# Optimization experiments

Hardware: AMD Instinct MI355X
Metric: run time of the kernel (lower is better)

## Reference

```python
import jax, jax.numpy as jnp
import numpy as np

SEQ_LEN, INPUT_DIM, HIDDEN, CLASSES, BATCH = 512, 512, 1024, 1000, 256


def _xavier(key, shape):
    fan_in, fan_out = shape
    limit = float(np.sqrt(6.0 / (fan_in + fan_out)))
    return jax.random.uniform(key, shape, jnp.float32, -limit, limit)


def setup_inputs() -> dict:
    key = jax.random.key(0)
    ks = jax.random.split(key, 10)
    inp = {
        "x": jax.random.normal(ks[0], (BATCH, INPUT_DIM, SEQ_LEN), jnp.float32),
        "W_fx": _xavier(ks[1], (INPUT_DIM, HIDDEN)),
        "W_fh": _xavier(ks[2], (HIDDEN, HIDDEN)),
        "W_gx": _xavier(ks[3], (INPUT_DIM, HIDDEN)),
        "W_gh": _xavier(ks[4], (HIDDEN, HIDDEN)),
        "W_ix": _xavier(ks[5], (INPUT_DIM, HIDDEN)),
        "W_ih": _xavier(ks[6], (HIDDEN, HIDDEN)),
        "W_ox": _xavier(ks[7], (INPUT_DIM, HIDDEN)),
        "W_oh": _xavier(ks[8], (HIDDEN, HIDDEN)),
        "W_ph": _xavier(ks[9], (HIDDEN, CLASSES)),
        "b_f": jnp.zeros((HIDDEN,), jnp.float32),
        "b_g": jnp.zeros((HIDDEN,), jnp.float32),
        "b_i": jnp.zeros((HIDDEN,), jnp.float32),
        "b_o": jnp.zeros((HIDDEN,), jnp.float32),
        "b_p": jnp.zeros((CLASSES,), jnp.float32),
    }
    return inp


def _lstm_forward(x, W_fx, W_fh, W_gx, W_gh, W_ix, W_ih, W_ox, W_oh,
                  W_ph, b_f, b_g, b_i, b_o, b_p):
    B, D, T = x.shape
    H = W_fh.shape[0]
    # Fuse the four input projections into one GEMM: [T, B, 4H]
    Wx = jnp.concatenate([W_gx, W_fx, W_ix, W_ox], axis=1)      # [D, 4H]
    Wh = jnp.concatenate([W_gh, W_fh, W_ih, W_oh], axis=1)      # [H, 4H]
    bias = jnp.concatenate([b_g, b_f, b_i, b_o])                # [4H]
    xt = jnp.transpose(x, (2, 0, 1))                            # [T, B, D]
    xproj = jnp.einsum('tbd,de->tbe', xt, Wx) + bias            # [T, B, 4H]

    def step(carry, xp):
        h, c = carry
        gates = jnp.tanh(h @ Wh + xp)                           # NOTE: source uses tanh for ALL gates
        g, f, i, o = jnp.split(gates, 4, axis=-1)
        c = g * i + c * f
        h = jnp.tanh(c) * o
        return (h, c), None

    h0 = jnp.zeros((B, H), x.dtype)
    c0 = jnp.zeros((B, H), x.dtype)
    (h, _), _ = jax.lax.scan(step, (h0, c0), xproj)
    return jax.nn.softmax(h @ W_ph + b_p, axis=-1)


def reference(x, W_fx, W_fh, W_gx, W_gh, W_ix, W_ih, W_ox, W_oh,
              W_ph, b_f, b_g, b_i, b_o, b_p):
    return _lstm_forward(x, W_fx, W_fh, W_gx, W_gh, W_ix, W_ih, W_ox, W_oh,
                         W_ph, b_f, b_g, b_i, b_o, b_p)
```

## Files before the change

### kernel.cpp

```cpp
#include <hip/hip_runtime.h>

#define B_SZ   256
#define D_IN   512
#define T_LEN  512
#define H_DIM  1024
#define KTOT   1536
#define NCLASS 1000

using half8   = __attribute__((ext_vector_type(8))) _Float16;
using floatx4 = __attribute__((ext_vector_type(4))) float;

__device__ __forceinline__ float ftanh(float x) {
    x = fminf(fmaxf(x, -20.f), 20.f);
    float e = __expf(2.f * x);
    return (e - 1.f) / (e + 1.f);
}

__global__ void k_transpose_x(const float* __restrict__ x, _Float16* __restrict__ xT) {
    __shared__ float tile[32][33];
    int b = blockIdx.z, d0 = blockIdx.y * 32, t0 = blockIdx.x * 32;
    int tx = threadIdx.x, ty = threadIdx.y;
    const float* xp = x + ((size_t)b * D_IN + d0) * T_LEN + t0;
#pragma unroll
    for (int i = 0; i < 4; ++i)
        tile[ty + i * 8][tx] = xp[(size_t)(ty + i * 8) * T_LEN + tx];
    __syncthreads();
#pragma unroll
    for (int i = 0; i < 4; ++i) {
        int t = t0 + ty + i * 8;
        xT[((size_t)t * B_SZ + b) * D_IN + d0 + tx] = (_Float16)tile[tx][ty + i * 8];
    }
}

__global__ void k_build_wcat(const float* __restrict__ Wgh, const float* __restrict__ Wfh,
                             const float* __restrict__ Wih, const float* __restrict__ Woh,
                             const float* __restrict__ Wgx, const float* __restrict__ Wfx,
                             const float* __restrict__ Wix, const float* __restrict__ Wox,
                             _Float16* __restrict__ WcatT) {
    int src = blockIdx.z;
    int kmax = (src < 4) ? 1024 : 512;
    int koff = (src < 4) ? 0 : 1024;
    int gi = src & 3;
    const float* W;
    switch (src) {
        case 0: W = Wgh; break; case 1: W = Wfh; break;
        case 2: W = Wih; break; case 3: W = Woh; break;
        case 4: W = Wgx; break; case 5: W = Wfx; break;
        case 6: W = Wix; break; default: W = Wox; break;
    }
    int k0 = blockIdx.y * 32;
    if (k0 >= kmax) return;
    int j0 = blockIdx.x * 32;
    __shared__ float tile[32][33];
    int tx = threadIdx.x, ty = threadIdx.y;
#pragma unroll
    for (int i = 0; i < 4; ++i)
        tile[ty + i * 8][tx] = W[(size_t)(k0 + ty + i * 8) * 1024 + j0 + tx];
    __syncthreads();
#pragma unroll
    for (int i = 0; i < 4; ++i) {
        int n = gi * 1024 + j0 + ty + i * 8;
        WcatT[(size_t)n * KTOT + koff + k0 + tx] = (_Float16)tile[tx][ty + i * 8];
    }
}

__global__ void k_init(float* __restrict__ c, unsigned int* __restrict__ h0u,
                       float* __restrict__ bias,
                       const float* __restrict__ bg, const float* __restrict__ bf,
                       const float* __restrict__ bi, const float* __restrict__ bo) {
    int idx = blockIdx.x * 256 + threadIdx.x;
    if (idx < 262144) c[idx] = 0.f;
    if (idx < 131072) h0u[idx] = 0u;
    if (idx < 4096) {
        int gi = idx >> 10, j = idx & 1023;
        float v = (gi == 0) ? bg[j] : (gi == 1) ? bf[j] : (gi == 2) ? bi[j] : bo[j];
        bias[idx] = v;
    }
}

__device__ __forceinline__ void bar() {
    asm volatile("s_waitcnt lgkmcnt(0)" ::: "memory");
    __builtin_amdgcn_s_barrier();
    asm volatile("" ::: "memory");
}

__global__ __launch_bounds__(256)
void k_step(const _Float16* __restrict__ h_in, _Float16* __restrict__ h_out,
            float* __restrict__ h_f32, float* __restrict__ c_st,
            const _Float16* __restrict__ xTt, const _Float16* __restrict__ WcatT,
            const float* __restrict__ bias, int is_last) {
    __shared__ __align__(16) _Float16 As[2][64][72];
    __shared__ __align__(16) _Float16 Bs[2][64][72];

    int bid = blockIdx.x;
    int xcd = bid & 7, idx = bid >> 3;
    int cg = xcd * 8 + (idx & 7);
    int rg = idx >> 3;
    int r0 = rg * 64, hc0 = cg * 16;

    int tid = threadIdx.x, wave = tid >> 6, lane = tid & 63;

    floatx4 acc[4];
#pragma unroll
    for (int g = 0; g < 4; ++g) acc[g] = (floatx4){0.f, 0.f, 0.f, 0.f};

    int arow = tid >> 2, ac16 = (tid & 3) << 4;
    const _Float16* hbase = h_in + (size_t)(r0 + arow) * H_DIM + ac16;
    const _Float16* xbase = xTt + (size_t)(r0 + arow) * D_IN + ac16;
    const _Float16* bbase = WcatT +
        (size_t)((arow >> 4) * 1024 + hc0 + (arow & 15)) * KTOT + ac16;

    int am = wave * 16 + (lane & 15);
    int koffA = (lane >> 4) << 3;
    int ncol = lane & 15;

#define LOADSET(A0, A1, B0, B1, c) do {                                         \
        const _Float16* _sa = ((c) < 16) ? (hbase + ((c) << 6))                 \
                                         : (xbase + (((c) - 16) << 6));         \
        A0 = ((const uint4*)_sa)[0]; A1 = ((const uint4*)_sa)[1];               \
        const _Float16* _sb = bbase + ((c) << 6);                               \
        B0 = ((const uint4*)_sb)[0]; B1 = ((const uint4*)_sb)[1];               \
    } while (0)

#define STORESET(A0, A1, B0, B1, buf) do {                                      \
        *(uint4*)&As[buf][arow][ac16]     = A0;                                 \
        *(uint4*)&As[buf][arow][ac16 + 8] = A1;                                 \
        *(uint4*)&Bs[buf][arow][ac16]     = B0;                                 \
        *(uint4*)&Bs[buf][arow][ac16 + 8] = B1;                                 \
    } while (0)

#define MFMA_CHUNK(buf) do {                                                    \
        _Pragma("unroll")                                                       \
        for (int kk = 0; kk < 2; ++kk) {                                        \
            half8 af = *(const half8*)&As[buf][am][kk * 32 + koffA];            \
            _Pragma("unroll")                                                   \
            for (int g = 0; g < 4; ++g) {                                       \
                half8 bf8 = *(const half8*)&Bs[buf][g * 16 + ncol][kk * 32 + koffA]; \
                acc[g] = __builtin_amdgcn_mfma_f32_16x16x32_f16(af, bf8, acc[g], 0, 0, 0); \
            }                                                                   \
        }                                                                       \
    } while (0)

    uint4 aA0, aA1, bA0, bA1;
    uint4 aB0, aB1, bB0, bB1;

    LOADSET(aA0, aA1, bA0, bA1, 0);
    LOADSET(aB0, aB1, bB0, bB1, 1);
    STORESET(aA0, aA1, bA0, bA1, 0);
    LOADSET(aA0, aA1, bA0, bA1, 2);
    bar();

#pragma unroll
    for (int cc = 0; cc < 12; ++cc) {
        STORESET(aB0, aB1, bB0, bB1, 1);
        MFMA_CHUNK(0);
        if (2 * cc + 3 < 24) LOADSET(aB0, aB1, bB0, bB1, 2 * cc + 3);
        bar();
        if (2 * cc + 2 < 24) STORESET(aA0, aA1, bA0, bA1, 0);
        MFMA_CHUNK(1);
        if (2 * cc + 4 < 24) LOADSET(aA0, aA1, bA0, bA1, 2 * cc + 4);
        bar();
    }

#undef LOADSET
#undef STORESET
#undef MFMA_CHUNK

    int q = lane >> 4, col = lane & 15;
    int gcol = hc0 + col;
    float bg_ = bias[gcol], bf_ = bias[1024 + gcol];
    float bi_ = bias[2048 + gcol], bo_ = bias[3072 + gcol];
#pragma unroll
    for (int r = 0; r < 4; ++r) {
        int grow = r0 + wave * 16 + q * 4 + r;
        size_t off = (size_t)grow * H_DIM + gcol;
        float g  = ftanh(acc[0][r] + bg_);
        float f  = ftanh(acc[1][r] + bf_);
        float ii = ftanh(acc[2][r] + bi_);
        float o  = ftanh(acc[3][r] + bo_);
        float cn = g * ii + c_st[off] * f;
        c_st[off] = cn;
        float hn = ftanh(cn) * o;
        h_out[off] = (_Float16)hn;
        if (is_last) h_f32[off] = hn;
    }
}

__global__ void k_logits(const float* __restrict__ h, const float* __restrict__ Wp,
                         const float* __restrict__ bp, float* __restrict__ logits) {
    __shared__ float hs[32][65];
    int r0 = blockIdx.y * 32;
    int c0 = blockIdx.x * 64;
    int tid = threadIdx.x;
    int wave = tid >> 6, tx = tid & 63;
    int col = c0 + tx;
    float s[8];
#pragma unroll
    for (int i = 0; i < 8; ++i) s[i] = 0.f;
    for (int kc = 0; kc < 16; ++kc) {
        int k0 = kc * 64;
#pragma unroll
        for (int i = 0; i < 8; ++i) {
            int idx = tid + i * 256;
            hs[idx >> 6][idx & 63] = h[(size_t)(r0 + (idx >> 6)) * H_DIM + k0 + (idx & 63)];
        }
        __syncthreads();
        if (col < NCLASS) {
            for (int kk = 0; kk < 64; ++kk) {
                float wv = Wp[(size_t)(k0 + kk) * NCLASS + col];
#pragma unroll
                for (int rr = 0; rr < 8; ++rr) s[rr] += hs[wave * 8 + rr][kk] * wv;
            }
        }
        __syncthreads();
    }
    if (col < NCLASS) {
#pragma unroll
        for (int rr = 0; rr < 8; ++rr)
            logits[(size_t)(r0 + wave * 8 + rr) * 1024 + col] = s[rr] + bp[col];
    }
}

__global__ void k_softmax(const float* __restrict__ logits, float* __restrict__ out) {
    __shared__ float red[256];
    int row = blockIdx.x, tid = threadIdx.x;
    float v[4];
    float mx = -1e30f;
#pragma unroll
    for (int i = 0; i < 4; ++i) {
        int c = tid + i * 256;
        float z = (c < NCLASS) ? logits[(size_t)row * 1024 + c] : -1e30f;
        v[i] = z;
        mx = fmaxf(mx, z);
    }
    red[tid] = mx; __syncthreads();
    for (int s = 128; s > 0; s >>= 1) {
        if (tid < s) red[tid] = fmaxf(red[tid], red[tid + s]);
        __syncthreads();
    }
    mx = red[0]; __syncthreads();
    float sum = 0.f;
#pragma unroll
    for (int i = 0; i < 4; ++i) {
        int c = tid + i * 256;
        v[i] = (c < NCLASS) ? __expf(v[i] - mx) : 0.f;
        sum += v[i];
    }
    red[tid] = sum; __syncthreads();
    for (int s = 128; s > 0; s >>= 1) {
        if (tid < s) red[tid] += red[tid + s];
        __syncthreads();
    }
    float inv = 1.f / red[0];
#pragma unroll
    for (int i = 0; i < 4; ++i) {
        int c = tid + i * 256;
        if (c < NCLASS) out[(size_t)row * NCLASS + c] = v[i] * inv;
    }
}

extern "C" void kernel_launch(void* const* d_in, const int* in_sizes, int n_in,
                              void* d_out, int out_size, void* d_ws, size_t ws_size,
                              hipStream_t stream) {
    const float* x   = (const float*)d_in[0];
    const float* Wfx = (const float*)d_in[1];
    const float* Wfh = (const float*)d_in[2];
    const float* Wgx = (const float*)d_in[3];
    const float* Wgh = (const float*)d_in[4];
    const float* Wix = (const float*)d_in[5];
    const float* Wih = (const float*)d_in[6];
    const float* Wox = (const float*)d_in[7];
    const float* Woh = (const float*)d_in[8];
    const float* Wph = (const float*)d_in[9];
    const float* bf  = (const float*)d_in[10];
    const float* bg  = (const float*)d_in[11];
    const float* bi  = (const float*)d_in[12];
    const float* bo  = (const float*)d_in[13];
    const float* bp  = (const float*)d_in[14];
    float* outp = (float*)d_out;

    char* ws = (char*)d_ws;
    _Float16* xT    = (_Float16*)(ws);
    _Float16* WcatT = (_Float16*)(ws + 134217728);
    float*    bias  = (float*)   (ws + 146800640);
    _Float16* hb0   = (_Float16*)(ws + 146817024);
    _Float16* hb1   = (_Float16*)(ws + 147341312);
    float*    c_st  = (float*)   (ws + 147865600);
    float*    hf32  = (float*)   (ws + 148914176);
    float*    logit = (float*)   (ws + 149962752);

    k_transpose_x<<<dim3(16, 16, 256), dim3(32, 8), 0, stream>>>(x, xT);
    k_build_wcat<<<dim3(32, 32, 8), dim3(32, 8), 0, stream>>>(
        Wgh, Wfh, Wih, Woh, Wgx, Wfx, Wix, Wox, WcatT);
    k_init<<<1024, 256, 0, stream>>>(c_st, (unsigned int*)hb0, bias, bg, bf, bi, bo);

    for (int t = 0; t < T_LEN; ++t) {
        const _Float16* hin = (t & 1) ? hb1 : hb0;
        _Float16*       hout = (t & 1) ? hb0 : hb1;
        k_step<<<256, 256, 0, stream>>>(hin, hout, hf32, c_st,
                                        xT + (size_t)t * B_SZ * D_IN, WcatT, bias,
                                        (t == T_LEN - 1) ? 1 : 0);
    }

    k_logits<<<dim3(16, 8), 256, 0, stream>>>(hf32, Wph, bp, logit);
    k_softmax<<<256, 256, 0, stream>>>(logit, outp);
}
```

Measured before the change: 5.949 ms.

## Use 32x32x16 MFMA with register-streamed weight fragments and LDS epilogue

```diff
diff --git a/kernel.cpp b/kernel.cpp
--- a/kernel.cpp
+++ b/kernel.cpp
@@ -7,8 +7,9 @@
 #define KTOT   1536
 #define NCLASS 1000
 
-using half8   = __attribute__((ext_vector_type(8))) _Float16;
-using floatx4 = __attribute__((ext_vector_type(4))) float;
+using half8    = __attribute__((ext_vector_type(8))) _Float16;
+using floatx4  = __attribute__((ext_vector_type(4))) float;
+using floatx16 = __attribute__((ext_vector_type(16))) float;
 
 __device__ __forceinline__ float ftanh(float x) {
     x = fminf(fmaxf(x, -20.f), 20.f);
@@ -90,7 +91,7 @@
             const _Float16* __restrict__ xTt, const _Float16* __restrict__ WcatT,
             const float* __restrict__ bias, int is_last) {
     __shared__ __align__(16) _Float16 As[2][64][72];
-    __shared__ __align__(16) _Float16 Bs[2][64][72];
+    __shared__ float eps[64][65];
 
     int bid = blockIdx.x;
     int xcd = bid & 7, idx = bid >> 3;
@@ -99,85 +100,98 @@
     int r0 = rg * 64, hc0 = cg * 16;
 
     int tid = threadIdx.x, wave = tid >> 6, lane = tid & 63;
-
-    floatx4 acc[4];
-#pragma unroll
-    for (int g = 0; g < 4; ++g) acc[g] = (floatx4){0.f, 0.f, 0.f, 0.f};
+    int rg2 = wave >> 1, gp = wave & 1;
+
+    floatx16 acc;
+#pragma unroll
+    for (int i = 0; i < 16; ++i) acc[i] = 0.f;
 
     int arow = tid >> 2, ac16 = (tid & 3) << 4;
     const _Float16* hbase = h_in + (size_t)(r0 + arow) * H_DIM + ac16;
     const _Float16* xbase = xTt + (size_t)(r0 + arow) * D_IN + ac16;
-    const _Float16* bbase = WcatT +
-        (size_t)((arow >> 4) * 1024 + hc0 + (arow & 15)) * KTOT + ac16;
-
-    int am = wave * 16 + (lane & 15);
-    int koffA = (lane >> 4) << 3;
-    int ncol = lane & 15;
-
-#define LOADSET(A0, A1, B0, B1, c) do {                                         \
+
+    int j = lane & 31;
+    int nrow = (gp * 2 + (j >> 4)) * 1024 + hc0 + (j & 15);
+    const _Float16* bptr = WcatT + (size_t)nrow * KTOT + ((lane >> 5) << 3);
+
+    int ard = rg2 * 32 + (lane & 31);
+    int akb = (lane >> 5) << 3;
+
+#define LOADA(A0, A1, c) do {                                                   \
         const _Float16* _sa = ((c) < 16) ? (hbase + ((c) << 6))                 \
                                          : (xbase + (((c) - 16) << 6));         \
         A0 = ((const uint4*)_sa)[0]; A1 = ((const uint4*)_sa)[1];               \
-        const _Float16* _sb = bbase + ((c) << 6);                               \
-        B0 = ((const uint4*)_sb)[0]; B1 = ((const uint4*)_sb)[1];               \
     } while (0)
 
-#define STORESET(A0, A1, B0, B1, buf) do {                                      \
+#define STOREA(A0, A1, buf) do {                                                \
         *(uint4*)&As[buf][arow][ac16]     = A0;                                 \
         *(uint4*)&As[buf][arow][ac16 + 8] = A1;                                 \
-        *(uint4*)&Bs[buf][arow][ac16]     = B0;                                 \
-        *(uint4*)&Bs[buf][arow][ac16 + 8] = B1;                                 \
     } while (0)
 
-#define MFMA_CHUNK(buf) do {                                                    \
+#define LOADB(S, c) do {                                                        \
+        S[0] = *(const half8*)(bptr + ((c) << 6));                              \
+        S[1] = *(const half8*)(bptr + ((c) << 6) + 16);                         \
+        S[2] = *(const half8*)(bptr + ((c) << 6) + 32);                         \
+        S[3] = *(const half8*)(bptr + ((c) << 6) + 48);                         \
+    } while (0)
+
+#define MFMA_CHUNK(buf, S) do {                                                 \
         _Pragma("unroll")                                                       \
-        for (int kk = 0; kk < 2; ++kk) {                                        \
-            half8 af = *(const half8*)&As[buf][am][kk * 32 + koffA];            \
-            _Pragma("unroll")                                                   \
-            for (int g = 0; g < 4; ++g) {                                       \
-                half8 bf8 = *(const half8*)&Bs[buf][g * 16 + ncol][kk * 32 + koffA]; \
-                acc[g] = __builtin_amdgcn_mfma_f32_16x16x32_f16(af, bf8, acc[g], 0, 0, 0); \
-            }                                                                   \
+        for (int ks = 0; ks < 4; ++ks) {                                        \
+            half8 af = *(const half8*)&As[buf][ard][ks * 16 + akb];             \
+            acc = __builtin_amdgcn_mfma_f32_32x32x16_f16(af, S[ks], acc, 0, 0, 0); \
         }                                                                       \
     } while (0)
 
-    uint4 aA0, aA1, bA0, bA1;
-    uint4 aB0, aB1, bB0, bB1;
-
-    LOADSET(aA0, aA1, bA0, bA1, 0);
-    LOADSET(aB0, aB1, bB0, bB1, 1);
-    STORESET(aA0, aA1, bA0, bA1, 0);
-    LOADSET(aA0, aA1, bA0, bA1, 2);
+    uint4 aE0, aE1, aO0, aO1;
+    half8 Bst[4][4];
+
+    LOADA(aE0, aE1, 0);
+    LOADA(aO0, aO1, 1);
+    LOADB(Bst[0], 0); LOADB(Bst[1], 1); LOADB(Bst[2], 2); LOADB(Bst[3], 3);
+    STOREA(aE0, aE1, 0);
+    LOADA(aE0, aE1, 2);
     bar();
 
 #pragma unroll
     for (int cc = 0; cc < 12; ++cc) {
-        STORESET(aB0, aB1, bB0, bB1, 1);
-        MFMA_CHUNK(0);
-        if (2 * cc + 3 < 24) LOADSET(aB0, aB1, bB0, bB1, 2 * cc + 3);
+        const int e = 2 * cc, o = e + 1;
+        STOREA(aO0, aO1, 1);
+        MFMA_CHUNK(0, Bst[e & 3]);
+        if (e + 4 < 24) LOADB(Bst[e & 3], e + 4);
+        if (o + 2 < 24) LOADA(aO0, aO1, o + 2);
         bar();
-        if (2 * cc + 2 < 24) STORESET(aA0, aA1, bA0, bA1, 0);
-        MFMA_CHUNK(1);
-        if (2 * cc + 4 < 24) LOADSET(aA0, aA1, bA0, bA1, 2 * cc + 4);
+        if (e + 2 < 24) STOREA(aE0, aE1, 0);
+        MFMA_CHUNK(1, Bst[o & 3]);
+        if (o + 4 < 24) LOADB(Bst[o & 3], o + 4);
+        if (e + 4 < 24) LOADA(aE0, aE1, e + 4);
         bar();
     }
 
-#undef LOADSET
-#undef STORESET
+#undef LOADA
+#undef STOREA
+#undef LOADB
 #undef MFMA_CHUNK
 
-    int q = lane >> 4, col = lane & 15;
-    int gcol = hc0 + col;
-    float bg_ = bias[gcol], bf_ = bias[1024 + gcol];
-    float bi_ = bias[2048 + gcol], bo_ = bias[3072 + gcol];
-#pragma unroll
-    for (int r = 0; r < 4; ++r) {
-        int grow = r0 + wave * 16 + q * 4 + r;
-        size_t off = (size_t)grow * H_DIM + gcol;
-        float g  = ftanh(acc[0][r] + bg_);
-        float f  = ftanh(acc[1][r] + bf_);
-        float ii = ftanh(acc[2][r] + bi_);
-        float o  = ftanh(acc[3][r] + bo_);
+#pragma unroll
+    for (int r = 0; r < 16; ++r) {
+        int row_m = ((lane >> 5) << 2) + (r & 3) + ((r >> 2) << 3);
+        eps[rg2 * 32 + row_m][(gp << 5) + j] = acc[r];
+    }
+    __syncthreads();
+
+    int hcol = tid & 15;
+    int rbase = (tid >> 4) << 2;
+    float bg_ = bias[hc0 + hcol],        bf_ = bias[1024 + hc0 + hcol];
+    float bi_ = bias[2048 + hc0 + hcol], bo_ = bias[3072 + hc0 + hcol];
+#pragma unroll
+    for (int rr = 0; rr < 4; ++rr) {
+        int row = rbase + rr;
+        size_t off = (size_t)(r0 + row) * H_DIM + hc0 + hcol;
+        float g  = ftanh(eps[row][hcol]      + bg_);
+        float f  = ftanh(eps[row][16 + hcol] + bf_);
+        float ii = ftanh(eps[row][32 + hcol] + bi_);
+        float o  = ftanh(eps[row][48 + hcol] + bo_);
         float cn = g * ii + c_st[off] * f;
         c_st[off] = cn;
         float hn = ftanh(cn) * o;
```

Measured after the change: 8.562 ms. 43.9% more time.
